# Performance work log

Hardware: AMD Instinct MI355X
Metric: run time of the kernel (lower is better)

## Reference

```python
import jax, jax.numpy as jnp
import numpy as np

N = 100000
E = 3200000
IN_C, HID, EMB = 128, 128, 64


def setup_inputs() -> dict:
    key = jax.random.key(0)
    ks = jax.random.split(key, 8)
    x = jax.random.normal(ks[0], (N, IN_C), dtype=jnp.float32)
    edge_index = jax.random.randint(ks[1], (2, E), 0, N, dtype=jnp.int64)
    def lin(k, out_c, in_c):
        s = 1.0 / np.sqrt(in_c)
        return jax.random.uniform(k, (out_c, in_c), jnp.float32, -s, s)
    # PyG SAGEConv: lin_l (applied to aggregated neighbors, has bias), lin_r (root, no bias)
    return {
        "x": x,
        "edge_index": edge_index,
        "Wl1": lin(ks[2], HID, IN_C), "bl1": jnp.zeros((HID,), jnp.float32), "Wr1": lin(ks[3], HID, IN_C),
        "Wl2": lin(ks[4], HID, HID), "bl2": jnp.zeros((HID,), jnp.float32), "Wr2": lin(ks[5], HID, HID),
        "Wl3": lin(ks[6], EMB, HID), "bl3": jnp.zeros((EMB,), jnp.float32), "Wr3": lin(ks[7], EMB, HID),
    }


def _sage(x, src, dst, Wl, bl, Wr):
    # mean-aggregate neighbor features onto destination nodes
    msg = x[src]                                           # [E, C] gather
    agg = jax.ops.segment_sum(msg, dst, num_segments=N)    # [N, C]
    cnt = jax.ops.segment_sum(jnp.ones((src.shape[0],), x.dtype), dst, num_segments=N)
    mean = agg / jnp.maximum(cnt, 1.0)[:, None]
    return mean @ Wl.T + bl + x @ Wr.T


def reference(x, edge_index, Wl1, bl1, Wr1, Wl2, bl2, Wr2, Wl3, bl3, Wr3):
    src, dst = edge_index[0], edge_index[1]
    h = jax.nn.relu(_sage(x, src, dst, Wl1, bl1, Wr1))
    h = jax.nn.relu(_sage(h, src, dst, Wl2, bl2, Wr2))
    return _sage(h, src, dst, Wl3, bl3, Wr3)
```

## Files before the change

### kernel.cpp

```cpp
#include <hip/hip_runtime.h>


#define NN 100000
#define CHUNK 8192
#define NBKT 512
#define NPOP 392
#define CAP 9664
#define PADCAP 3584
#define STRIDE (CAP + PADCAP)

typedef _Float16 half_t;
typedef __attribute__((ext_vector_type(4))) _Float16 half4v;
typedef __attribute__((ext_vector_type(8))) _Float16 half8v;
typedef __attribute__((ext_vector_type(4))) float float4v;
typedef __attribute__((ext_vector_type(2))) float float2v;
typedef __attribute__((ext_vector_type(4))) unsigned int uint4v;

__global__ __launch_bounds__(512) void init_misc(half_t* __restrict__ xh,
                                                 half_t* __restrict__ hh,
                                                 unsigned char* __restrict__ xq,
                                                 int* __restrict__ cfill) {
    constexpr size_t SLAB32 = (size_t)(NN + 1) * 32;
    constexpr size_t SLAB64B = (size_t)(NN + 1) * 64;
    int t = threadIdx.x;
    cfill[t] = t * CAP;
    if (t < 256) {
        int sel = t >> 7;
        int cg = (t >> 5) & 3;
        int c = t & 31;
        half_t* p = sel ? hh : xh;
        p[(size_t)cg * SLAB32 + (size_t)NN * 32 + c] = (half_t)0.f;
    }
    if (t < 32) {
        int cg = t >> 4;
        int i = t & 15;
        ((unsigned int*)(xq + (size_t)cg * SLAB64B + (size_t)NN * 64))[i] = 0u;
    }
}

__global__ __launch_bounds__(256) void partition_kernel(const int* __restrict__ src,
                                                        const int* __restrict__ dst,
                                                        int* __restrict__ cfill,
                                                        unsigned int* __restrict__ coarse,
                                                        int E) {
    __shared__ int h[NBKT];
    __shared__ int off[NBKT];
    __shared__ int tsum[256];
    __shared__ unsigned int stage[CHUNK];
    int tid = threadIdx.x;
    h[2 * tid] = 0;
    h[2 * tid + 1] = 0;
    __syncthreads();
    int base = blockIdx.x * CHUNK;
    int nE = min(CHUNK, E - base);
    for (int i = tid; i < nE; i += 256) atomicAdd(&h[dst[base + i] >> 8], 1);
    __syncthreads();
    int c0 = h[2 * tid], c1 = h[2 * tid + 1];
    tsum[tid] = c0 + c1;
    __syncthreads();
    for (int o = 1; o < 256; o <<= 1) {
        int v = (tid >= o) ? tsum[tid - o] : 0;
        __syncthreads();
        tsum[tid] += v;
        __syncthreads();
    }
    int run = (tid == 0) ? 0 : tsum[tid - 1];
    off[2 * tid] = run;
    off[2 * tid + 1] = run + c0;
    __syncthreads();
    for (int i = tid; i < nE; i += 256) {
        int d = dst[base + i];
        int s_ = src[base + i];
        int bin = d >> 8;
        int pos = atomicAdd(&off[bin], 1);
        stage[pos] = ((unsigned)(d & 255) << 17) | (unsigned)s_;
    }
    __syncthreads();
#pragma unroll
    for (int jj = 0; jj < 2; jj++) {
        int bin = 2 * tid + jj;
        int c = h[bin];
        if (c) {
            int gs = atomicAdd(&cfill[bin], c);
            int lim = bin * CAP + CAP;
            int cc = min(c, max(0, lim - gs));
            int lstart = off[bin] - c;
            for (int k = 0; k < cc; k++) coarse[gs + k] = stage[lstart + k];
        }
    }
}

__global__ __launch_bounds__(256) void fine_sort_kernel(const unsigned int* __restrict__ coarse,
                                                        const int* __restrict__ cfill,
                                                        int* __restrict__ pbeg,
                                                        int* __restrict__ pend,
                                                        float* __restrict__ invdeg,
                                                        int* __restrict__ sorted_src, int n) {
    __shared__ int fh[512];
    __shared__ int foff[512];
    __shared__ int cur[512];
    __shared__ int tsum[256];
    int b = blockIdx.x;
    int beg = b * CAP;
    int end = min(cfill[b], beg + CAP);
    int nb = end - beg;
    int tid = threadIdx.x;
    fh[2 * tid] = 0;
    fh[2 * tid + 1] = 0;
    __syncthreads();
    for (int i = tid; i < nb; i += 256) {
        unsigned p = coarse[beg + i];
        int f = (int)((p >> 17) << 1) | ((p & 0x1FFFF) >= (NN / 2) ? 1 : 0);
        atomicAdd(&fh[f], 1);
    }
    __syncthreads();
    int b0 = tid * 2;
    int pcs[2];
    int s = 0;
#pragma unroll
    for (int j = 0; j < 2; j++) {
        int pc = (fh[b0 + j] + 7) & ~7;
        pcs[j] = pc;
        s += pc;
    }
    tsum[tid] = s;
    __syncthreads();
    for (int o = 1; o < 256; o <<= 1) {
        int v = (tid >= o) ? tsum[tid - o] : 0;
        __syncthreads();
        tsum[tid] += v;
        __syncthreads();
    }
    int run = (tid == 0) ? 0 : tsum[tid - 1];
    int pbase = b * STRIDE;
#pragma unroll
    for (int j = 0; j < 2; j++) {
        int ln = b0 + j;
        int rbeg = pbase + run;
        foff[ln] = run;
        cur[ln] = rbeg;
        int node = b * 256 + (ln >> 1);
        if (node < n) {
            pbeg[2 * node + (ln & 1)] = rbeg;
            pend[2 * node + (ln & 1)] = rbeg + pcs[j];
        }
        run += pcs[j];
    }
    __syncthreads();
    for (int i = tid; i < nb; i += 256) {
        unsigned p = coarse[beg + i];
        int f = (int)((p >> 17) << 1) | ((p & 0x1FFFF) >= (NN / 2) ? 1 : 0);
        int pos = atomicAdd(&cur[f], 1);
        sorted_src[pos] = (int)(p & 0x1FFFF);
    }
#pragma unroll
    for (int j = 0; j < 2; j++) {
        int ln = b0 + j;
        int raw = fh[ln];
        int rbeg = pbase + foff[ln];
        for (int k = raw; k < pcs[j]; k++) sorted_src[rbeg + k] = NN;
    }
    int nd = b * 256 + tid;
    if (nd < n) {
        int d = fh[2 * tid] + fh[2 * tid + 1];
        invdeg[nd] = d > 0 ? 1.0f / (float)d : 0.0f;
    }
}

__global__ void cast_f2h(const float* __restrict__ in, half_t* __restrict__ out,
                         unsigned char* __restrict__ xq, int n4) {
    constexpr size_t SLAB32 = (size_t)(NN + 1) * 32;
    constexpr size_t SLAB64B = (size_t)(NN + 1) * 64;
    int t = blockIdx.x * blockDim.x + threadIdx.x;
    if (t < n4) {
        float4 v = *(const float4*)(in + (size_t)t * 4);
        half4v r = {(half_t)v.x, (half_t)v.y, (half_t)v.z, (half_t)v.w};
        int e = t * 4;
        int node = e >> 7;
        int c = e & 127;
        *(half4v*)(out + (size_t)(c >> 5) * SLAB32 + (size_t)node * 32 + (c & 31)) = r;
        unsigned int q = __builtin_amdgcn_cvt_pk_fp8_f32(v.x, v.y, 0, false);
        q = __builtin_amdgcn_cvt_pk_fp8_f32(v.z, v.w, q, true);
        *(unsigned int*)(xq + (size_t)(c >> 6) * SLAB64B + (size_t)node * 64 + (c & 63)) = q;
    }
}

template <int C_IN, int C_OUT>
__device__ inline void prep_one(const float* __restrict__ W, half_t* __restrict__ B, int t) {
    constexpr int NCT = C_OUT / 16;
    if (t >= C_IN * C_OUT) return;
    int jj = t & 7;
    int kq = (t >> 3) & 3;
    int c = (t >> 5) & 15;
    int ct = (t >> 9) % NCT;
    int chunk = t / (512 * NCT);
    int k = chunk * 32 + kq * 8 + jj;
    int j = ct * 16 + c;
    B[t] = (half_t)W[(size_t)j * C_IN + k];
}

__global__ __launch_bounds__(256) void prep_all(
    const float* __restrict__ Wl1, const float* __restrict__ Wr1,
    const float* __restrict__ Wl2, const float* __restrict__ Wr2,
    const float* __restrict__ Wl3, const float* __restrict__ Wr3,
    half_t* Bl1, half_t* Br1, half_t* Bl2, half_t* Br2, half_t* Bl3, half_t* Br3) {
    int b = blockIdx.x;
    int tid = threadIdx.x;
    if (b < 256) {
        int sel = b >> 6;
        int t = (b & 63) * 256 + tid;
        const float* W = sel == 0 ? Wl1 : sel == 1 ? Wr1 : sel == 2 ? Wl2 : Wr2;
        half_t* B = sel == 0 ? Bl1 : sel == 1 ? Br1 : sel == 2 ? Bl2 : Br2;
        prep_one<128, 128>(W, B, t);
    } else {
        int idx = b - 256;
        int sel = idx >> 5;
        int t = (idx & 31) * 256 + tid;
        prep_one<128, 64>(sel == 0 ? Wl3 : Wr3, sel == 0 ? Bl3 : Br3, t);
    }
}

__device__ inline void acc16(float* a, uint4v w) {
#pragma unroll
    for (int j = 0; j < 4; j++) {
        float2v lo = __builtin_amdgcn_cvt_pk_f32_fp8(w[j], false);
        float2v hi = __builtin_amdgcn_cvt_pk_f32_fp8(w[j], true);
        a[4 * j + 0] += lo.x;
        a[4 * j + 1] += lo.y;
        a[4 * j + 2] += hi.x;
        a[4 * j + 3] += hi.y;
    }
}

__global__ __launch_bounds__(256) void gather_q128(
    const unsigned char* __restrict__ xq,
    const int* __restrict__ pbeg, const int* __restrict__ pend,
    const int* __restrict__ sorted_src, const float* __restrict__ invdeg,
    half_t* __restrict__ part0,
    half_t* __restrict__ part1,
    int n) {
    constexpr size_t SLAB64B = (size_t)(NN + 1) * 64;
    int slice = blockIdx.x & 3;
    int cg = slice >> 1;
    int s = slice & 1;
    int tid = threadIdx.x;
    int node = (blockIdx.x >> 2) * 32 + (tid >> 3);
    if (node >= n) return;
    int slot = (tid >> 2) & 1;
    int col = tid & 3;
    const char* bp = (const char*)xq + (size_t)cg * SLAB64B + (unsigned)(col << 4);
    int beg = pbeg[2 * node + s];
    int end = pend[2 * node + s];
    float a[16];
#pragma unroll
    for (int i = 0; i < 16; i++) a[i] = 0.f;
    int j = beg + slot;
    if (j < end) {
        int s0 = sorted_src[j];
        int s1 = sorted_src[j + 2];
        int s2 = sorted_src[j + 4];
        int s3 = sorted_src[j + 6];
        for (j += 8; j < end; j += 8) {
            int t0 = sorted_src[j];
            int t1 = sorted_src[j + 2];
            int t2 = sorted_src[j + 4];
            int t3 = sorted_src[j + 6];
            uint4v w0 = *(const uint4v*)(bp + ((unsigned)s0 << 6));
            uint4v w1 = *(const uint4v*)(bp + ((unsigned)s1 << 6));
            uint4v w2 = *(const uint4v*)(bp + ((unsigned)s2 << 6));
            uint4v w3 = *(const uint4v*)(bp + ((unsigned)s3 << 6));
            acc16(a, w0); acc16(a, w1); acc16(a, w2); acc16(a, w3);
            s0 = t0; s1 = t1; s2 = t2; s3 = t3;
        }
        uint4v w0 = *(const uint4v*)(bp + ((unsigned)s0 << 6));
        uint4v w1 = *(const uint4v*)(bp + ((unsigned)s1 << 6));
        uint4v w2 = *(const uint4v*)(bp + ((unsigned)s2 << 6));
        uint4v w3 = *(const uint4v*)(bp + ((unsigned)s3 << 6));
        acc16(a, w0); acc16(a, w1); acc16(a, w2); acc16(a, w3);
    }
#pragma unroll
    for (int i = 0; i < 16; i++) a[i] += __shfl_xor(a[i], 4);
    if (slot == 0) {
        float iv = invdeg[node];
        half8v r0, r1;
#pragma unroll
        for (int i = 0; i < 8; i++) {
            r0[i] = (half_t)(a[i] * iv);
            r1[i] = (half_t)(a[8 + i] * iv);
        }
        half_t* pp = (s == 0 ? part0 : part1) + (size_t)node * 128 + cg * 64 + col * 16;
        __builtin_nontemporal_store(r0, (half8v*)pp);
        __builtin_nontemporal_store(r1, (half8v*)(pp + 8));
    }
}

__global__ __launch_bounds__(256) void gather_part128(
    const half_t* __restrict__ feat,
    const int* __restrict__ pbeg, const int* __restrict__ pend,
    const int* __restrict__ sorted_src, const float* __restrict__ invdeg,
    half_t* __restrict__ part0, half_t* __restrict__ part1, int n) {
    constexpr size_t SLAB32 = (size_t)(NN + 1) * 32;
    int slice = blockIdx.x & 7;
    int cg = slice >> 1;
    int s = slice & 1;
    int tid = threadIdx.x;
    int node = (blockIdx.x >> 3) * 32 + (tid >> 3);
    if (node >= n) return;
    int slot = (tid >> 2) & 1;
    int col = tid & 3;
    const char* bp = (const char*)feat + (size_t)cg * SLAB32 * 2 + (unsigned)(col << 4);
    int beg = pbeg[2 * node + s];
    int end = pend[2 * node + s];
    float a0 = 0.f, a1 = 0.f, a2 = 0.f, a3 = 0.f, a4 = 0.f, a5 = 0.f, a6 = 0.f, a7 = 0.f;
    int j = beg + slot;
    if (j < end) {
        int s0 = sorted_src[j];
        int s1 = sorted_src[j + 2];
        int s2 = sorted_src[j + 4];
        int s3 = sorted_src[j + 6];
        for (j += 8; j < end; j += 8) {
            int t0 = sorted_src[j];
            int t1 = sorted_src[j + 2];
            int t2 = sorted_src[j + 4];
            int t3 = sorted_src[j + 6];
            half8v v0 = *(const half8v*)(bp + ((unsigned)s0 << 6));
            half8v v1 = *(const half8v*)(bp + ((unsigned)s1 << 6));
            half8v v2 = *(const half8v*)(bp + ((unsigned)s2 << 6));
            half8v v3 = *(const half8v*)(bp + ((unsigned)s3 << 6));
            a0 += ((float)v0[0] + (float)v1[0]) + ((float)v2[0] + (float)v3[0]);
            a1 += ((float)v0[1] + (float)v1[1]) + ((float)v2[1] + (float)v3[1]);
            a2 += ((float)v0[2] + (float)v1[2]) + ((float)v2[2] + (float)v3[2]);
            a3 += ((float)v0[3] + (float)v1[3]) + ((float)v2[3] + (float)v3[3]);
            a4 += ((float)v0[4] + (float)v1[4]) + ((float)v2[4] + (float)v3[4]);
            a5 += ((float)v0[5] + (float)v1[5]) + ((float)v2[5] + (float)v3[5]);
            a6 += ((float)v0[6] + (float)v1[6]) + ((float)v2[6] + (float)v3[6]);
            a7 += ((float)v0[7] + (float)v1[7]) + ((float)v2[7] + (float)v3[7]);
            s0 = t0; s1 = t1; s2 = t2; s3 = t3;
        }
        half8v v0 = *(const half8v*)(bp + ((unsigned)s0 << 6));
        half8v v1 = *(const half8v*)(bp + ((unsigned)s1 << 6));
        half8v v2 = *(const half8v*)(bp + ((unsigned)s2 << 6));
        half8v v3 = *(const half8v*)(bp + ((unsigned)s3 << 6));
        a0 += ((float)v0[0] + (float)v1[0]) + ((float)v2[0] + (float)v3[0]);
        a1 += ((float)v0[1] + (float)v1[1]) + ((float)v2[1] + (float)v3[1]);
        a2 += ((float)v0[2] + (float)v1[2]) + ((float)v2[2] + (float)v3[2]);
        a3 += ((float)v0[3] + (float)v1[3]) + ((float)v2[3] + (float)v3[3]);
        a4 += ((float)v0[4] + (float)v1[4]) + ((float)v2[4] + (float)v3[4]);
        a5 += ((float)v0[5] + (float)v1[5]) + ((float)v2[5] + (float)v3[5]);
        a6 += ((float)v0[6] + (float)v1[6]) + ((float)v2[6] + (float)v3[6]);
        a7 += ((float)v0[7] + (float)v1[7]) + ((float)v2[7] + (float)v3[7]);
    }
    a0 += __shfl_xor(a0, 4); a1 += __shfl_xor(a1, 4);
    a2 += __shfl_xor(a2, 4); a3 += __shfl_xor(a3, 4);
    a4 += __shfl_xor(a4, 4); a5 += __shfl_xor(a5, 4);
    a6 += __shfl_xor(a6, 4); a7 += __shfl_xor(a7, 4);
    if (slot == 0) {
        float iv = invdeg[node];
        half8v r = {(half_t)(a0 * iv), (half_t)(a1 * iv), (half_t)(a2 * iv), (half_t)(a3 * iv),
                    (half_t)(a4 * iv), (half_t)(a5 * iv), (half_t)(a6 * iv), (half_t)(a7 * iv)};
        half_t* pp = (s == 0 ? part0 : part1);
        __builtin_nontemporal_store(r, (half8v*)(pp + (size_t)node * 128 + cg * 32 + col * 8));
    }
}

__global__ __launch_bounds__(256) void gather_part64(
    const half_t* __restrict__ z,
    const int* __restrict__ pbeg, const int* __restrict__ pend,
    const int* __restrict__ sorted_src, const float* __restrict__ invdeg,
    half_t* __restrict__ part0, half_t* __restrict__ part1, int n) {
    constexpr size_t SLAB32 = (size_t)(NN + 1) * 32;
    int slice = blockIdx.x & 3;
    int hg = slice >> 1;
    int s = slice & 1;
    int tid = threadIdx.x;
    int node = (blockIdx.x >> 2) * 32 + (tid >> 3);
    if (node >= n) return;
    int slot = (tid >> 2) & 1;
    int col = tid & 3;
    const char* bp = (const char*)z + (size_t)hg * SLAB32 * 2 + (unsigned)(col << 4);
    int beg = pbeg[2 * node + s];
    int end = pend[2 * node + s];
    float a0 = 0.f, a1 = 0.f, a2 = 0.f, a3 = 0.f, a4 = 0.f, a5 = 0.f, a6 = 0.f, a7 = 0.f;
    int j = beg + slot;
    if (j < end) {
        int s0 = sorted_src[j];
        int s1 = sorted_src[j + 2];
        int s2 = sorted_src[j + 4];
        int s3 = sorted_src[j + 6];
        for (j += 8; j < end; j += 8) {
            int t0 = sorted_src[j];
            int t1 = sorted_src[j + 2];
            int t2 = sorted_src[j + 4];
            int t3 = sorted_src[j + 6];
            half8v v0 = *(const half8v*)(bp + ((unsigned)s0 << 6));
            half8v v1 = *(const half8v*)(bp + ((unsigned)s1 << 6));
            half8v v2 = *(const half8v*)(bp + ((unsigned)s2 << 6));
            half8v v3 = *(const half8v*)(bp + ((unsigned)s3 << 6));
            a0 += ((float)v0[0] + (float)v1[0]) + ((float)v2[0] + (float)v3[0]);
            a1 += ((float)v0[1] + (float)v1[1]) + ((float)v2[1] + (float)v3[1]);
            a2 += ((float)v0[2] + (float)v1[2]) + ((float)v2[2] + (float)v3[2]);
            a3 += ((float)v0[3] + (float)v1[3]) + ((float)v2[3] + (float)v3[3]);
            a4 += ((float)v0[4] + (float)v1[4]) + ((float)v2[4] + (float)v3[4]);
            a5 += ((float)v0[5] + (float)v1[5]) + ((float)v2[5] + (float)v3[5]);
            a6 += ((float)v0[6] + (float)v1[6]) + ((float)v2[6] + (float)v3[6]);
            a7 += ((float)v0[7] + (float)v1[7]) + ((float)v2[7] + (float)v3[7]);
            s0 = t0; s1 = t1; s2 = t2; s3 = t3;
        }
        half8v v0 = *(const half8v*)(bp + ((unsigned)s0 << 6));
        half8v v1 = *(const half8v*)(bp + ((unsigned)s1 << 6));
        half8v v2 = *(const half8v*)(bp + ((unsigned)s2 << 6));
        half8v v3 = *(const half8v*)(bp + ((unsigned)s3 << 6));
        a0 += ((float)v0[0] + (float)v1[0]) + ((float)v2[0] + (float)v3[0]);
        a1 += ((float)v0[1] + (float)v1[1]) + ((float)v2[1] + (float)v3[1]);
        a2 += ((float)v0[2] + (float)v1[2]) + ((float)v2[2] + (float)v3[2]);
        a3 += ((float)v0[3] + (float)v1[3]) + ((float)v2[3] + (float)v3[3]);
        a4 += ((float)v0[4] + (float)v1[4]) + ((float)v2[4] + (float)v3[4]);
        a5 += ((float)v0[5] + (float)v1[5]) + ((float)v2[5] + (float)v3[5]);
        a6 += ((float)v0[6] + (float)v1[6]) + ((float)v2[6] + (float)v3[6]);
        a7 += ((float)v0[7] + (float)v1[7]) + ((float)v2[7] + (float)v3[7]);
    }
    a0 += __shfl_xor(a0, 4); a1 += __shfl_xor(a1, 4);
    a2 += __shfl_xor(a2, 4); a3 += __shfl_xor(a3, 4);
    a4 += __shfl_xor(a4, 4); a5 += __shfl_xor(a5, 4);
    a6 += __shfl_xor(a6, 4); a7 += __shfl_xor(a7, 4);
    if (slot == 0) {
        float iv = invdeg[node];
        half8v r = {(half_t)(a0 * iv), (half_t)(a1 * iv), (half_t)(a2 * iv), (half_t)(a3 * iv),
                    (half_t)(a4 * iv), (half_t)(a5 * iv), (half_t)(a6 * iv), (half_t)(a7 * iv)};
        half_t* pp = (s == 0 ? part0 : part1);
        __builtin_nontemporal_store(r, (half8v*)(pp + (size_t)node * 64 + hg * 32 + col * 8));
    }
}

__device__ inline half8v load_a32(const half_t* __restrict__ A, int rowc, int q, int ch) {
    constexpr size_t SLAB32 = (size_t)(NN + 1) * 32;
    return *(const half8v*)(A + (size_t)ch * SLAB32 + (size_t)rowc * 32 + q * 8);
}

template <bool FUSE_Z>
__global__ __launch_bounds__(256) void mfma_layer128(
    const half_t* __restrict__ rootSl,
    const half_t* __restrict__ part0, const half_t* __restrict__ part1,
    const half_t* __restrict__ Bl, const half_t* __restrict__ Br,
    const float* __restrict__ bias, half_t* __restrict__ outSl,
    const half_t* __restrict__ Bz, half_t* __restrict__ z_out, int n) {
    constexpr int NCT = 8;
    constexpr size_t SLAB32 = (size_t)(NN + 1) * 32;
    __shared__ __align__(16) half_t tile[4][16][136];
    int tid = threadIdx.x;
    int w = tid >> 6;
    int l = tid & 63;
    int c = l & 15;
    int q = l >> 4;
    int row = blockIdx.x * 64 + w * 16 + c;
    int rowc = min(row, n - 1);

    float4v acc[NCT];
#pragma unroll
    for (int i = 0; i < NCT; i++) acc[i] = (float4v){0.f, 0.f, 0.f, 0.f};

    {
        const half_t* B = Bl + (size_t)(c * 4 + q) * 8;
#pragma unroll
        for (int ch = 0; ch < 4; ch++) {
            half8v p0 = *(const half8v*)(part0 + (size_t)rowc * 128 + ch * 32 + q * 8);
            half8v p1 = *(const half8v*)(part1 + (size_t)rowc * 128 + ch * 32 + q * 8);
            half8v a = p0 + p1;
            half8v b[NCT];
#pragma unroll
            for (int t2 = 0; t2 < NCT; t2++)
                b[t2] = *(const half8v*)(B + (size_t)ch * (NCT * 512) + t2 * 512);
#pragma unroll
            for (int t2 = 0; t2 < NCT; t2++)
                acc[t2] = __builtin_amdgcn_mfma_f32_16x16x32_f16(a, b[t2], acc[t2], 0, 0, 0);
        }
    }
    {
        const half_t* B = Br + (size_t)(c * 4 + q) * 8;
#pragma unroll
        for (int ch = 0; ch < 4; ch++) {
            half8v a = load_a32(rootSl, rowc, q, ch);
            half8v b[NCT];
#pragma unroll
            for (int t2 = 0; t2 < NCT; t2++)
                b[t2] = *(const half8v*)(B + (size_t)ch * (NCT * 512) + t2 * 512);
#pragma unroll
            for (int t2 = 0; t2 < NCT; t2++)
                acc[t2] = __builtin_amdgcn_mfma_f32_16x16x32_f16(a, b[t2], acc[t2], 0, 0, 0);
        }
    }

    half_t (*T)[136] = tile[w];
    int lr0 = q * 4;
#pragma unroll
    for (int t2 = 0; t2 < NCT; t2++) {
        float bv = bias[t2 * 16 + c];
#pragma unroll
        for (int r = 0; r < 4; r++)
            T[lr0 + r][t2 * 16 + c] = (half_t)fmaxf(acc[t2][r] + bv, 0.f);
    }
    __syncthreads();

    int srow = l >> 2;
    int piece = l & 3;
    int grow = blockIdx.x * 64 + w * 16 + srow;
    if (grow < n) {
#pragma unroll
        for (int s = 0; s < 4; s++) {
            half8v v = *(const half8v*)(&T[srow][s * 32 + piece * 8]);
            *(half8v*)(outSl + (size_t)s * SLAB32 + (size_t)grow * 32 + piece * 8) = v;
        }
    }

    if (FUSE_Z) {
        float4v accz[4];
#pragma unroll
        for (int i = 0; i < 4; i++) accz[i] = (float4v){0.f, 0.f, 0.f, 0.f};
        const half_t* B = Bz + (size_t)(c * 4 + q) * 8;
#pragma unroll
        for (int ch = 0; ch < 4; ch++) {
            half8v a = *(const half8v*)(&T[c][ch * 32 + q * 8]);
            half8v b[4];
#pragma unroll
            for (int t2 = 0; t2 < 4; t2++)
                b[t2] = *(const half8v*)(B + (size_t)ch * (4 * 512) + t2 * 512);
#pragma unroll
            for (int t2 = 0; t2 < 4; t2++)
                accz[t2] = __builtin_amdgcn_mfma_f32_16x16x32_f16(a, b[t2], accz[t2], 0, 0, 0);
        }
#pragma unroll
        for (int t2 = 0; t2 < 4; t2++)
#pragma unroll
            for (int r = 0; r < 4; r++)
                T[lr0 + r][t2 * 16 + c] = (half_t)accz[t2][r];
        if (grow < n) {
#pragma unroll
            for (int s = 0; s < 2; s++) {
                half8v v = *(const half8v*)(&T[srow][s * 32 + piece * 8]);
                *(half8v*)(z_out + (size_t)s * SLAB32 + (size_t)grow * 32 + piece * 8) = v;
            }
        }
    }
}

__global__ __launch_bounds__(256) void mfma_final(
    const half_t* __restrict__ A_sl, const half_t* __restrict__ Bp,
    const half_t* __restrict__ pz0, const half_t* __restrict__ pz1,
    const float* __restrict__ bias, float* __restrict__ out, int n) {
    constexpr int NCT = 4;
    __shared__ __align__(16) float Tf[4][16][68];
    int tid = threadIdx.x;
    int w = tid >> 6;
    int l = tid & 63;
    int c = l & 15;
    int q = l >> 4;
    int row = blockIdx.x * 64 + w * 16 + c;
    int rowc = min(row, n - 1);

    float4v acc[NCT];
#pragma unroll
    for (int i = 0; i < NCT; i++) acc[i] = (float4v){0.f, 0.f, 0.f, 0.f};

    const half_t* B = Bp + (size_t)(c * 4 + q) * 8;
#pragma unroll
    for (int ch = 0; ch < 4; ch++) {
        half8v a = load_a32(A_sl, rowc, q, ch);
        half8v b[NCT];
#pragma unroll
        for (int t2 = 0; t2 < NCT; t2++)
            b[t2] = *(const half8v*)(B + (size_t)ch * (NCT * 512) + t2 * 512);
#pragma unroll
        for (int t2 = 0; t2 < NCT; t2++)
            acc[t2] = __builtin_amdgcn_mfma_f32_16x16x32_f16(a, b[t2], acc[t2], 0, 0, 0);
    }

#pragma unroll
    for (int t2 = 0; t2 < NCT; t2++) {
        float bv = bias[t2 * 16 + c];
#pragma unroll
        for (int r = 0; r < 4; r++)
            Tf[w][q * 4 + r][t2 * 16 + c] = acc[t2][r] + bv;
    }
    __syncthreads();

    int row16 = l >> 2;
    int piece = l & 3;
    int grow = blockIdx.x * 64 + w * 16 + row16;
    if (grow < n) {
        const half_t* z0 = pz0 + (size_t)grow * 64 + piece * 16;
        const half_t* z1 = pz1 + (size_t)grow * 64 + piece * 16;
        half8v p0a = *(const half8v*)z0;
        half8v p0b = *(const half8v*)(z0 + 8);
        half8v p1a = *(const half8v*)z1;
        half8v p1b = *(const half8v*)(z1 + 8);
        float vals[16];
#pragma unroll
        for (int i = 0; i < 8; i++)
            vals[i] = Tf[w][row16][piece * 16 + i] + (float)p0a[i] + (float)p1a[i];
#pragma unroll
        for (int i = 0; i < 8; i++)
            vals[8 + i] = Tf[w][row16][piece * 16 + 8 + i] + (float)p0b[i] + (float)p1b[i];
        float* op = out + (size_t)grow * 64 + piece * 16;
#pragma unroll
        for (int k = 0; k < 4; k++) {
            float4 o = {vals[4 * k], vals[4 * k + 1], vals[4 * k + 2], vals[4 * k + 3]};
            *(float4*)(op + k * 4) = o;
        }
    }
}

extern "C" void kernel_launch(void* const* d_in, const int* in_sizes, int n_in,
                              void* d_out, int out_size, void* d_ws, size_t ws_size,
                              hipStream_t stream) {
    const float* x   = (const float*)d_in[0];
    const int*   ei  = (const int*)d_in[1];
    const float* Wl1 = (const float*)d_in[2];
    const float* bl1 = (const float*)d_in[3];
    const float* Wr1 = (const float*)d_in[4];
    const float* Wl2 = (const float*)d_in[5];
    const float* bl2 = (const float*)d_in[6];
    const float* Wr2 = (const float*)d_in[7];
    const float* Wl3 = (const float*)d_in[8];
    const float* bl3 = (const float*)d_in[9];
    const float* Wr3 = (const float*)d_in[10];

    const int N = NN;
    const int E = in_sizes[1] / 2;
    const int* src = ei;
    const int* dst = ei + E;

    const size_t SLABSZ = (size_t)(NN + 1) * 32;
    const size_t SLAB64B = (size_t)(NN + 1) * 64;

    char* ws = (char*)d_ws;
    half_t* xh_sl = (half_t*)ws;
    half_t* hh_sl = xh_sl + 4 * SLABSZ;
    half_t* part0 = hh_sl + 4 * SLABSZ;
    half_t* part1 = part0 + (size_t)N * 128;
    half_t* z_grp  = xh_sl;
    half_t* partz0 = part0;
    half_t* partz1 = part1;
    unsigned char* xq = (unsigned char*)(part1 + (size_t)N * 128);
    int* cfill    = (int*)(xq + 2 * SLAB64B);
    int* pbeg     = cfill + 512;
    int* pend     = pbeg + 2 * N + 256;
    float* invdeg = (float*)(pend + 2 * N + 256);
    unsigned int* coarse = (unsigned int*)(invdeg + N);
    int* sorted_src = (int*)(coarse + (size_t)NPOP * CAP);
    half_t* Bl1 = (half_t*)(sorted_src + (size_t)NPOP * STRIDE + 64);
    half_t* Br1 = Bl1 + 128 * 128;
    half_t* Bl2 = Br1 + 128 * 128;
    half_t* Br2 = Bl2 + 128 * 128;
    half_t* Bl3 = Br2 + 128 * 128;
    half_t* Br3 = Bl3 + 64 * 128;

    cast_f2h<<<(N * 128 / 4 + 255) / 256, 256, 0, stream>>>(x, xh_sl, xq, N * 128 / 4);
    prep_all<<<320, 256, 0, stream>>>(Wl1, Wr1, Wl2, Wr2, Wl3, Wr3,
                                      Bl1, Br1, Bl2, Br2, Bl3, Br3);
    init_misc<<<1, 512, 0, stream>>>(xh_sl, hh_sl, xq, cfill);

    const int sort_blocks = (E + CHUNK - 1) / CHUNK;
    partition_kernel<<<sort_blocks, 256, 0, stream>>>(src, dst, cfill, coarse, E);
    fine_sort_kernel<<<(N + 255) / 256, 256, 0, stream>>>(coarse, cfill, pbeg, pend,
                                                          invdeg, sorted_src, N);

    const int gq_blocks   = ((N + 31) / 32) * 4;
    const int g128_blocks = ((N + 31) / 32) * 8;
    const int g64_blocks  = ((N + 31) / 32) * 4;
    const int gemm_blocks = (N + 63) / 64;

    gather_q128<<<gq_blocks, 256, 0, stream>>>(xq, pbeg, pend, sorted_src,
                                               invdeg, part0, part1, N);
    mfma_layer128<false><<<gemm_blocks, 256, 0, stream>>>(
        xh_sl, part0, part1, Bl1, Br1, bl1, hh_sl, nullptr, nullptr, N);

    gather_part128<<<g128_blocks, 256, 0, stream>>>(hh_sl, pbeg, pend, sorted_src,
                                                    invdeg, part0, part1, N);
    mfma_layer128<true><<<gemm_blocks, 256, 0, stream>>>(
        hh_sl, part0, part1, Bl2, Br2, bl2, hh_sl, Bl3, z_grp, N);

    gather_part64<<<g64_blocks, 256, 0, stream>>>(z_grp, pbeg, pend, sorted_src,
                                                  invdeg, partz0, partz1, N);
    mfma_final<<<gemm_blocks, 256, 0, stream>>>(hh_sl, Br3, partz0, partz1,
                                                bl3, (float*)d_out, N);
}
```

Before: 493.1 us.

## Gather layer-2 and layer-3 neighbor features from FP8 copies instead of FP16

The layer GEMM epilogues now also write FP8-packed copies of the hidden activations (hq) and of the projected z features (zq). The layer-2 and layer-3 neighbor gathers read these FP8 copies, reusing gather_q128 and a new gather_q64, in place of the FP16 gathers. This halves the bytes fetched per random neighbor row, which is the dominant memory cost of the aggregation. In exchange it adds FP8 conversion and store work to the GEMM epilogues and loses precision in the aggregated means.

New measurement: 452.7 us. 8.2% less time.

```diff
diff --git a/kernel.cpp b/kernel.cpp
--- a/kernel.cpp
+++ b/kernel.cpp
@@ -19,6 +19,7 @@
 __global__ __launch_bounds__(512) void init_misc(half_t* __restrict__ xh,
                                                  half_t* __restrict__ hh,
                                                  unsigned char* __restrict__ xq,
+                                                 unsigned char* __restrict__ hq,
                                                  int* __restrict__ cfill) {
     constexpr size_t SLAB32 = (size_t)(NN + 1) * 32;
     constexpr size_t SLAB64B = (size_t)(NN + 1) * 64;
@@ -31,10 +32,12 @@
         half_t* p = sel ? hh : xh;
         p[(size_t)cg * SLAB32 + (size_t)NN * 32 + c] = (half_t)0.f;
     }
-    if (t < 32) {
-        int cg = t >> 4;
+    if (t < 64) {
+        int sel = t >> 5;
+        int cg = (t >> 4) & 1;
         int i = t & 15;
-        ((unsigned int*)(xq + (size_t)cg * SLAB64B + (size_t)NN * 64))[i] = 0u;
+        unsigned char* p = sel ? hq : xq;
+        ((unsigned int*)(p + (size_t)cg * SLAB64B + (size_t)NN * 64))[i] = 0u;
     }
 }
 
@@ -294,24 +297,25 @@
     }
 }
 
-__global__ __launch_bounds__(256) void gather_part128(
-    const half_t* __restrict__ feat,
+__global__ __launch_bounds__(256) void gather_q64(
+    const unsigned char* __restrict__ zq,
     const int* __restrict__ pbeg, const int* __restrict__ pend,
     const int* __restrict__ sorted_src, const float* __restrict__ invdeg,
-    half_t* __restrict__ part0, half_t* __restrict__ part1, int n) {
-    constexpr size_t SLAB32 = (size_t)(NN + 1) * 32;
-    int slice = blockIdx.x & 7;
-    int cg = slice >> 1;
-    int s = slice & 1;
+    half_t* __restrict__ part0,
+    half_t* __restrict__ part1,
+    int n) {
+    int s = blockIdx.x & 1;
     int tid = threadIdx.x;
-    int node = (blockIdx.x >> 3) * 32 + (tid >> 3);
+    int node = (blockIdx.x >> 1) * 32 + (tid >> 3);
     if (node >= n) return;
     int slot = (tid >> 2) & 1;
     int col = tid & 3;
-    const char* bp = (const char*)feat + (size_t)cg * SLAB32 * 2 + (unsigned)(col << 4);
+    const char* bp = (const char*)zq + (unsigned)(col << 4);
     int beg = pbeg[2 * node + s];
     int end = pend[2 * node + s];
-    float a0 = 0.f, a1 = 0.f, a2 = 0.f, a3 = 0.f, a4 = 0.f, a5 = 0.f, a6 = 0.f, a7 = 0.f;
+    float a[16];
+#pragma unroll
+    for (int i = 0; i < 16; i++) a[i] = 0.f;
     int j = beg + slot;
     if (j < end) {
         int s0 = sorted_src[j];
@@ -323,118 +327,49 @@
             int t1 = sorted_src[j + 2];
             int t2 = sorted_src[j + 4];
             int t3 = sorted_src[j + 6];
-            half8v v0 = *(const half8v*)(bp + ((unsigned)s0 << 6));
-            half8v v1 = *(const half8v*)(bp + ((unsigned)s1 << 6));
-            half8v v2 = *(const half8v*)(bp + ((unsigned)s2 << 6));
-            half8v v3 = *(const half8v*)(bp + ((unsigned)s3 << 6));
-            a0 += ((float)v0[0] + (float)v1[0]) + ((float)v2[0] + (float)v3[0]);
-            a1 += ((float)v0[1] + (float)v1[1]) + ((float)v2[1] + (float)v3[1]);
-            a2 += ((float)v0[2] + (float)v1[2]) + ((float)v2[2] + (float)v3[2]);
-            a3 += ((float)v0[3] + (float)v1[3]) + ((float)v2[3] + (float)v3[3]);
-            a4 += ((float)v0[4] + (float)v1[4]) + ((float)v2[4] + (float)v3[4]);
-            a5 += ((float)v0[5] + (float)v1[5]) + ((float)v2[5] + (float)v3[5]);
-            a6 += ((float)v0[6] + (float)v1[6]) + ((float)v2[6] + (float)v3[6]);
-            a7 += ((float)v0[7] + (float)v1[7]) + ((float)v2[7] + (float)v3[7]);
+            uint4v w0 = *(const uint4v*)(bp + ((unsigned)s0 << 6));
+            uint4v w1 = *(const uint4v*)(bp + ((unsigned)s1 << 6));
+            uint4v w2 = *(const uint4v*)(bp + ((unsigned)s2 << 6));
+            uint4v w3 = *(const uint4v*)(bp + ((unsigned)s3 << 6));
+            acc16(a, w0); acc16(a, w1); acc16(a, w2); acc16(a, w3);
             s0 = t0; s1 = t1; s2 = t2; s3 = t3;
         }
-        half8v v0 = *(const half8v*)(bp + ((unsigned)s0 << 6));
-        half8v v1 = *(const half8v*)(bp + ((unsigned)s1 << 6));
-        half8v v2 = *(const half8v*)(bp + ((unsigned)s2 << 6));
-        half8v v3 = *(const half8v*)(bp + ((unsigned)s3 << 6));
-        a0 += ((float)v0[0] + (float)v1[0]) + ((float)v2[0] + (float)v3[0]);
-        a1 += ((float)v0[1] + (float)v1[1]) + ((float)v2[1] + (float)v3[1]);
-        a2 += ((float)v0[2] + (float)v1[2]) + ((float)v2[2] + (float)v3[2]);
-        a3 += ((float)v0[3] + (float)v1[3]) + ((float)v2[3] + (float)v3[3]);
-        a4 += ((float)v0[4] + (float)v1[4]) + ((float)v2[4] + (float)v3[4]);
-        a5 += ((float)v0[5] + (float)v1[5]) + ((float)v2[5] + (float)v3[5]);
-        a6 += ((float)v0[6] + (float)v1[6]) + ((float)v2[6] + (float)v3[6]);
-        a7 += ((float)v0[7] + (float)v1[7]) + ((float)v2[7] + (float)v3[7]);
-    }
-    a0 += __shfl_xor(a0, 4); a1 += __shfl_xor(a1, 4);
-    a2 += __shfl_xor(a2, 4); a3 += __shfl_xor(a3, 4);
-    a4 += __shfl_xor(a4, 4); a5 += __shfl_xor(a5, 4);
-    a6 += __shfl_xor(a6, 4); a7 += __shfl_xor(a7, 4);
+        uint4v w0 = *(const uint4v*)(bp + ((unsigned)s0 << 6));
+        uint4v w1 = *(const uint4v*)(bp + ((unsigned)s1 << 6));
+        uint4v w2 = *(const uint4v*)(bp + ((unsigned)s2 << 6));
+        uint4v w3 = *(const uint4v*)(bp + ((unsigned)s3 << 6));
+        acc16(a, w0); acc16(a, w1); acc16(a, w2); acc16(a, w3);
+    }
+#pragma unroll
+    for (int i = 0; i < 16; i++) a[i] += __shfl_xor(a[i], 4);
     if (slot == 0) {
         float iv = invdeg[node];
-        half8v r = {(half_t)(a0 * iv), (half_t)(a1 * iv), (half_t)(a2 * iv), (half_t)(a3 * iv),
-                    (half_t)(a4 * iv), (half_t)(a5 * iv), (half_t)(a6 * iv), (half_t)(a7 * iv)};
-        half_t* pp = (s == 0 ? part0 : part1);
-        __builtin_nontemporal_store(r, (half8v*)(pp + (size_t)node * 128 + cg * 32 + col * 8));
-    }
-}
-
-__global__ __launch_bounds__(256) void gather_part64(
-    const half_t* __restrict__ z,
-    const int* __restrict__ pbeg, const int* __restrict__ pend,
-    const int* __restrict__ sorted_src, const float* __restrict__ invdeg,
-    half_t* __restrict__ part0, half_t* __restrict__ part1, int n) {
-    constexpr size_t SLAB32 = (size_t)(NN + 1) * 32;
-    int slice = blockIdx.x & 3;
-    int hg = slice >> 1;
-    int s = slice & 1;
-    int tid = threadIdx.x;
-    int node = (blockIdx.x >> 2) * 32 + (tid >> 3);
-    if (node >= n) return;
-    int slot = (tid >> 2) & 1;
-    int col = tid & 3;
-    const char* bp = (const char*)z + (size_t)hg * SLAB32 * 2 + (unsigned)(col << 4);
-    int beg = pbeg[2 * node + s];
-    int end = pend[2 * node + s];
-    float a0 = 0.f, a1 = 0.f, a2 = 0.f, a3 = 0.f, a4 = 0.f, a5 = 0.f, a6 = 0.f, a7 = 0.f;
-    int j = beg + slot;
-    if (j < end) {
-        int s0 = sorted_src[j];
-        int s1 = sorted_src[j + 2];
-        int s2 = sorted_src[j + 4];
-        int s3 = sorted_src[j + 6];
-        for (j += 8; j < end; j += 8) {
-            int t0 = sorted_src[j];
-            int t1 = sorted_src[j + 2];
-            int t2 = sorted_src[j + 4];
-            int t3 = sorted_src[j + 6];
-            half8v v0 = *(const half8v*)(bp + ((unsigned)s0 << 6));
-            half8v v1 = *(const half8v*)(bp + ((unsigned)s1 << 6));
-            half8v v2 = *(const half8v*)(bp + ((unsigned)s2 << 6));
-            half8v v3 = *(const half8v*)(bp + ((unsigned)s3 << 6));
-            a0 += ((float)v0[0] + (float)v1[0]) + ((float)v2[0] + (float)v3[0]);
-            a1 += ((float)v0[1] + (float)v1[1]) + ((float)v2[1] + (float)v3[1]);
-            a2 += ((float)v0[2] + (float)v1[2]) + ((float)v2[2] + (float)v3[2]);
-            a3 += ((float)v0[3] + (float)v1[3]) + ((float)v2[3] + (float)v3[3]);
-            a4 += ((float)v0[4] + (float)v1[4]) + ((float)v2[4] + (float)v3[4]);
-            a5 += ((float)v0[5] + (float)v1[5]) + ((float)v2[5] + (float)v3[5]);
-            a6 += ((float)v0[6] + (float)v1[6]) + ((float)v2[6] + (float)v3[6]);
-            a7 += ((float)v0[7] + (float)v1[7]) + ((float)v2[7] + (float)v3[7]);
-            s0 = t0; s1 = t1; s2 = t2; s3 = t3;
-        }
-        half8v v0 = *(const half8v*)(bp + ((unsigned)s0 << 6));
-        half8v v1 = *(const half8v*)(bp + ((unsigned)s1 << 6));
-        half8v v2 = *(const half8v*)(bp + ((unsigned)s2 << 6));
-        half8v v3 = *(const half8v*)(bp + ((unsigned)s3 << 6));
-        a0 += ((float)v0[0] + (float)v1[0]) + ((float)v2[0] + (float)v3[0]);
-        a1 += ((float)v0[1] + (float)v1[1]) + ((float)v2[1] + (float)v3[1]);
-        a2 += ((float)v0[2] + (float)v1[2]) + ((float)v2[2] + (float)v3[2]);
-        a3 += ((float)v0[3] + (float)v1[3]) + ((float)v2[3] + (float)v3[3]);
-        a4 += ((float)v0[4] + (float)v1[4]) + ((float)v2[4] + (float)v3[4]);
-        a5 += ((float)v0[5] + (float)v1[5]) + ((float)v2[5] + (float)v3[5]);
-        a6 += ((float)v0[6] + (float)v1[6]) + ((float)v2[6] + (float)v3[6]);
-        a7 += ((float)v0[7] + (float)v1[7]) + ((float)v2[7] + (float)v3[7]);
-    }
-    a0 += __shfl_xor(a0, 4); a1 += __shfl_xor(a1, 4);
-    a2 += __shfl_xor(a2, 4); a3 += __shfl_xor(a3, 4);
-    a4 += __shfl_xor(a4, 4); a5 += __shfl_xor(a5, 4);
-    a6 += __shfl_xor(a6, 4); a7 += __shfl_xor(a7, 4);
-    if (slot == 0) {
-        float iv = invdeg[node];
-        half8v r = {(half_t)(a0 * iv), (half_t)(a1 * iv), (half_t)(a2 * iv), (half_t)(a3 * iv),
-                    (half_t)(a4 * iv), (half_t)(a5 * iv), (half_t)(a6 * iv), (half_t)(a7 * iv)};
-        half_t* pp = (s == 0 ? part0 : part1);
-        __builtin_nontemporal_store(r, (half8v*)(pp + (size_t)node * 64 + hg * 32 + col * 8));
+        half8v r0, r1;
+#pragma unroll
+        for (int i = 0; i < 8; i++) {
+            r0[i] = (half_t)(a[i] * iv);
+            r1[i] = (half_t)(a[8 + i] * iv);
+        }
+        half_t* pp = (s == 0 ? part0 : part1) + (size_t)node * 64 + col * 16;
+        __builtin_nontemporal_store(r0, (half8v*)pp);
+        __builtin_nontemporal_store(r1, (half8v*)(pp + 8));
     }
 }
 
 __device__ inline half8v load_a32(const half_t* __restrict__ A, int rowc, int q, int ch) {
     constexpr size_t SLAB32 = (size_t)(NN + 1) * 32;
     return *(const half8v*)(A + (size_t)ch * SLAB32 + (size_t)rowc * 32 + q * 8);
+}
+
+__device__ inline uint4v pack16(const half_t* tp) {
+    uint4v qv;
+#pragma unroll
+    for (int g = 0; g < 4; g++) {
+        unsigned q = __builtin_amdgcn_cvt_pk_fp8_f32((float)tp[g * 4], (float)tp[g * 4 + 1], 0, false);
+        q = __builtin_amdgcn_cvt_pk_fp8_f32((float)tp[g * 4 + 2], (float)tp[g * 4 + 3], q, true);
+        qv[g] = q;
+    }
+    return qv;
 }
 
 template <bool FUSE_Z>
@@ -443,9 +378,11 @@
     const half_t* __restrict__ part0, const half_t* __restrict__ part1,
     const half_t* __restrict__ Bl, const half_t* __restrict__ Br,
     const float* __restrict__ bias, half_t* __restrict__ outSl,
-    const half_t* __restrict__ Bz, half_t* __restrict__ z_out, int n) {
+    unsigned char* __restrict__ hq,
+    const half_t* __restrict__ Bz, unsigned char* __restrict__ zq, int n) {
     constexpr int NCT = 8;
     constexpr size_t SLAB32 = (size_t)(NN + 1) * 32;
+    constexpr size_t SLAB64B = (size_t)(NN + 1) * 64;
     __shared__ __align__(16) half_t tile[4][16][136];
     int tid = threadIdx.x;
     int w = tid >> 6;
@@ -510,6 +447,11 @@
             half8v v = *(const half8v*)(&T[srow][s * 32 + piece * 8]);
             *(half8v*)(outSl + (size_t)s * SLAB32 + (size_t)grow * 32 + piece * 8) = v;
         }
+#pragma unroll
+        for (int pl = 0; pl < 2; pl++) {
+            uint4v qv = pack16(&T[srow][pl * 64 + piece * 16]);
+            *(uint4v*)(hq + (size_t)pl * SLAB64B + (size_t)grow * 64 + piece * 16) = qv;
+        }
     }
 
     if (FUSE_Z) {
@@ -534,11 +476,8 @@
             for (int r = 0; r < 4; r++)
                 T[lr0 + r][t2 * 16 + c] = (half_t)accz[t2][r];
         if (grow < n) {
-#pragma unroll
-            for (int s = 0; s < 2; s++) {
-                half8v v = *(const half8v*)(&T[srow][s * 32 + piece * 8]);
-                *(half8v*)(z_out + (size_t)s * SLAB32 + (size_t)grow * 32 + piece * 8) = v;
-            }
+            uint4v qv = pack16(&T[srow][piece * 16]);
+            *(uint4v*)(zq + (size_t)grow * 64 + piece * 16) = qv;
         }
     }
 }
@@ -637,11 +576,12 @@
     half_t* hh_sl = xh_sl + 4 * SLABSZ;
     half_t* part0 = hh_sl + 4 * SLABSZ;
     half_t* part1 = part0 + (size_t)N * 128;
-    half_t* z_grp  = xh_sl;
     half_t* partz0 = part0;
     half_t* partz1 = part1;
     unsigned char* xq = (unsigned char*)(part1 + (size_t)N * 128);
-    int* cfill    = (int*)(xq + 2 * SLAB64B);
+    unsigned char* zq = xq;
+    unsigned char* hq = xq + 2 * SLAB64B;
+    int* cfill    = (int*)(hq + 2 * SLAB64B);
     int* pbeg     = cfill + 512;
     int* pend     = pbeg + 2 * N + 256;
     float* invdeg = (float*)(pend + 2 * N + 256);
@@ -657,30 +597,29 @@
     cast_f2h<<<(N * 128 / 4 + 255) / 256, 256, 0, stream>>>(x, xh_sl, xq, N * 128 / 4);
     prep_all<<<320, 256, 0, stream>>>(Wl1, Wr1, Wl2, Wr2, Wl3, Wr3,
                                       Bl1, Br1, Bl2, Br2, Bl3, Br3);
-    init_misc<<<1, 512, 0, stream>>>(xh_sl, hh_sl, xq, cfill);
+    init_misc<<<1, 512, 0, stream>>>(xh_sl, hh_sl, xq, hq, cfill);
 
     const int sort_blocks = (E + CHUNK - 1) / CHUNK;
     partition_kernel<<<sort_blocks, 256, 0, stream>>>(src, dst, cfill, coarse, E);
     fine_sort_kernel<<<(N + 255) / 256, 256, 0, stream>>>(coarse, cfill, pbeg, pend,
                                                           invdeg, sorted_src, N);
 
-    const int gq_blocks   = ((N + 31) / 32) * 4;
-    const int g128_blocks = ((N + 31) / 32) * 8;
-    const int g64_blocks  = ((N + 31) / 32) * 4;
+    const int gq_blocks  = ((N + 31) / 32) * 4;
+    const int gz_blocks  = ((N + 31) / 32) * 2;
     const int gemm_blocks = (N + 63) / 64;
 
     gather_q128<<<gq_blocks, 256, 0, stream>>>(xq, pbeg, pend, sorted_src,
                                                invdeg, part0, part1, N);
     mfma_layer128<false><<<gemm_blocks, 256, 0, stream>>>(
-        xh_sl, part0, part1, Bl1, Br1, bl1, hh_sl, nullptr, nullptr, N);
-
-    gather_part128<<<g128_blocks, 256, 0, stream>>>(hh_sl, pbeg, pend, sorted_src,
-                                                    invdeg, part0, part1, N);
+        xh_sl, part0, part1, Bl1, Br1, bl1, hh_sl, hq, nullptr, nullptr, N);
+
+    gather_q128<<<gq_blocks, 256, 0, stream>>>(hq, pbeg, pend, sorted_src,
+                                               invdeg, part0, part1, N);
     mfma_layer128<true><<<gemm_blocks, 256, 0, stream>>>(
-        hh_sl, part0, part1, Bl2, Br2, bl2, hh_sl, Bl3, z_grp, N);
-
-    gather_part64<<<g64_blocks, 256, 0, stream>>>(z_grp, pbeg, pend, sorted_src,
-                                                  invdeg, partz0, partz1, N);
+        hh_sl, part0, part1, Bl2, Br2, bl2, hh_sl, hq, Bl3, zq, N);
+
+    gather_q64<<<gz_blocks, 256, 0, stream>>>(zq, pbeg, pend, sorted_src,
+                                              invdeg, partz0, partz1, N);
     mfma_final<<<gemm_blocks, 256, 0, stream>>>(hh_sl, Br3, partz0, partz1,
                                                 bl3, (float*)d_out, N);
 }
```
